# Performance work log

Measured on AMD Instinct MI355X. Metric: run time of the kernel, lower is better.

## Reference

```python
import jax, jax.numpy as jnp
import numpy as np

FP8_MAX = 448.0  # torch.finfo(float8_e4m3fn).max

def _fp8_round(v):
    # round-to-nearest fp8 e4m3fn, back to f32 (simulated quantization)
    return v.astype(jnp.float8_e4m3fn).astype(jnp.float32)

def setup_inputs() -> dict:
    key = jax.random.key(0)
    k_x, k_w, k_b = jax.random.split(key, 3)
    M, K, N = 8, 8192, 8192
    x = jax.random.normal(k_x, (M, K), dtype=jnp.float32)
    w = jax.random.normal(k_w, (K, N), dtype=jnp.float32) * 0.02
    # per-output-column weight quantization (amax-to-scale)
    w_amax = jnp.max(jnp.abs(w), axis=0)                      # [N]
    w_scale = jnp.where(w_amax > 0, FP8_MAX / w_amax, 1.0)    # [N]
    weight_fp8_t = _fp8_round(w * w_scale[None, :])           # [K, N] fp8 values in f32
    weight_scale_inv = (1.0 / w_scale).astype(jnp.float32)    # [N]
    bias = jax.random.normal(k_b, (N,), dtype=jnp.float32) * 0.01
    return {"x": x, "weight_fp8_t": weight_fp8_t,
            "weight_scale_inv": weight_scale_inv, "bias": bias}

def reference(x, weight_fp8_t, weight_scale_inv, bias):
    # dynamic per-row activation quantization: amax -> scale
    amax = jnp.max(jnp.abs(x), axis=-1)                       # [M]
    x_scale = jnp.where(amax > 0, FP8_MAX / amax, 1.0)        # [M]
    x_fp8 = _fp8_round(x * x_scale[:, None])                  # [M, K]
    # scaled matmul: acc * x_scale_inv * weight_scale_inv (per row / per col)
    acc = jnp.einsum('mk,kn->mn', x_fp8, weight_fp8_t)        # [M, N]
    y = acc * (1.0 / x_scale)[:, None] * weight_scale_inv[None, :]
    return y + bias[None, :]
```

## Files before the change

kernel.cpp:

```cpp
#include <hip/hip_runtime.h>
#include <stdint.h>

#define MM 8
#define KK 8192
#define NN 8192
#define KC 256
#define KSPLIT (KK / KC)
#define FP8MAXV 448.0f

typedef float f32x4 __attribute__((ext_vector_type(4)));
typedef float f32x2 __attribute__((ext_vector_type(2)));

#define XQT_OFF 64
#define PART_OFF (XQT_OFF + KK * MM)

__device__ __forceinline__ float fp8_e4m3_round(float v) {
    uint32_t u = __float_as_uint(v);
    uint32_t mag = u & 0x7fffffffu;
    if (mag >= 0x3C800000u) {
        uint32_t lsb = (u >> 20) & 1u;
        uint32_t r = u + 0x0007FFFFu + lsb;
        r &= 0xFFF00000u;
        return __uint_as_float(r);
    }
    return rintf(v * 512.0f) * (1.0f / 512.0f);
}

__global__ __launch_bounds__(256) void prep_kernel(const float* __restrict__ x,
                                                   float* __restrict__ ws) {
    const int m = blockIdx.x;
    const int tid = threadIdx.x;
    const float* row = x + (size_t)m * KK;

    float amax = 0.0f;
    for (int k = tid * 4; k < KK; k += 256 * 4) {
        f32x4 v = *(const f32x4*)(row + k);
        amax = fmaxf(amax, fmaxf(fmaxf(fabsf(v.x), fabsf(v.y)),
                                 fmaxf(fabsf(v.z), fabsf(v.w))));
    }
#pragma unroll
    for (int off = 32; off >= 1; off >>= 1)
        amax = fmaxf(amax, __shfl_xor(amax, off, 64));

    __shared__ float sred[4];
    __shared__ float sscale;
    if ((tid & 63) == 0) sred[tid >> 6] = amax;
    __syncthreads();
    if (tid == 0) {
        float a = fmaxf(fmaxf(sred[0], sred[1]), fmaxf(sred[2], sred[3]));
        float scale = (a > 0.0f) ? (FP8MAXV / a) : 1.0f;
        sscale = scale;
        ws[m] = 1.0f / scale;
    }
    __syncthreads();
    const float scale = sscale;

    float* xqT = ws + XQT_OFF;
    for (int k = tid; k < KK; k += 256)
        xqT[(size_t)k * MM + m] = fp8_e4m3_round(row[k] * scale);
}

__global__ __launch_bounds__(256, 4) void gemm_partial(const float* __restrict__ W,
                                                       const float* __restrict__ wsinv,
                                                       const float* __restrict__ ws,
                                                       float* __restrict__ part) {
    const int n  = blockIdx.x * 256 + threadIdx.x;
    const int c  = blockIdx.y;
    const int k0 = c * KC;

    __shared__ float sxq[KC * MM];
    {
        const f32x4* src = (const f32x4*)(ws + XQT_OFF + (size_t)k0 * MM);
        ((f32x4*)sxq)[threadIdx.x]       = src[threadIdx.x];
        ((f32x4*)sxq)[threadIdx.x + 256] = src[threadIdx.x + 256];
    }
    __syncthreads();

    f32x2 acc[4];
#pragma unroll
    for (int i = 0; i < 4; ++i) acc[i] = (f32x2)0.0f;

    const float* Wp = W + (size_t)k0 * NN + n;
#pragma unroll 8
    for (int k = 0; k < KC; ++k) {
        float w = Wp[(size_t)k * NN];
        const f32x2* a2 = (const f32x2*)(sxq + k * MM);
        acc[0] += a2[0] * w;
        acc[1] += a2[1] * w;
        acc[2] += a2[2] * w;
        acc[3] += a2[3] * w;
    }

    const float wsn = wsinv[n];
    float* p = part + ((size_t)c * MM) * NN + n;
#pragma unroll
    for (int i = 0; i < 4; ++i) {
        p[(size_t)(2 * i + 0) * NN] = acc[i].x * (ws[2 * i + 0] * wsn);
        p[(size_t)(2 * i + 1) * NN] = acc[i].y * (ws[2 * i + 1] * wsn);
    }
}

__global__ __launch_bounds__(256) void reduce_kernel(const float* __restrict__ part,
                                                     const float* __restrict__ bias,
                                                     float* __restrict__ out) {
    const int idx = blockIdx.x * 256 + threadIdx.x;
    float s = bias[idx & (NN - 1)];
#pragma unroll
    for (int c = 0; c < KSPLIT; ++c)
        s += part[(size_t)c * MM * NN + idx];
    out[idx] = s;
}

__global__ __launch_bounds__(256) void init_kernel(const float* __restrict__ bias,
                                                   float* __restrict__ out) {
    int idx = blockIdx.x * 256 + threadIdx.x;
    out[idx] = bias[idx & (NN - 1)];
}

__global__ __launch_bounds__(256, 4) void gemm_atomic(const float* __restrict__ W,
                                                      const float* __restrict__ wsinv,
                                                      const float* __restrict__ ws,
                                                      float* __restrict__ out) {
    const int n  = blockIdx.x * 256 + threadIdx.x;
    const int k0 = blockIdx.y * KC;

    __shared__ float sxq[KC * MM];
    {
        const f32x4* src = (const f32x4*)(ws + XQT_OFF + (size_t)k0 * MM);
        ((f32x4*)sxq)[threadIdx.x]       = src[threadIdx.x];
        ((f32x4*)sxq)[threadIdx.x + 256] = src[threadIdx.x + 256];
    }
    __syncthreads();

    f32x2 acc[4];
#pragma unroll
    for (int i = 0; i < 4; ++i) acc[i] = (f32x2)0.0f;

    const float* Wp = W + (size_t)k0 * NN + n;
#pragma unroll 8
    for (int k = 0; k < KC; ++k) {
        float w = Wp[(size_t)k * NN];
        const f32x2* a2 = (const f32x2*)(sxq + k * MM);
        acc[0] += a2[0] * w;
        acc[1] += a2[1] * w;
        acc[2] += a2[2] * w;
        acc[3] += a2[3] * w;
    }

    const float wsn = wsinv[n];
#pragma unroll
    for (int i = 0; i < 4; ++i) {
        unsafeAtomicAdd(out + (size_t)(2 * i + 0) * NN + n, acc[i].x * (ws[2 * i + 0] * wsn));
        unsafeAtomicAdd(out + (size_t)(2 * i + 1) * NN + n, acc[i].y * (ws[2 * i + 1] * wsn));
    }
}

extern "C" void kernel_launch(void* const* d_in, const int* in_sizes, int n_in,
                              void* d_out, int out_size, void* d_ws, size_t ws_size,
                              hipStream_t stream) {
    const float* x     = (const float*)d_in[0];
    const float* W     = (const float*)d_in[1];
    const float* wsinv = (const float*)d_in[2];
    const float* bias  = (const float*)d_in[3];
    float* out = (float*)d_out;
    float* ws  = (float*)d_ws;

    const size_t need = (size_t)(PART_OFF + (size_t)KSPLIT * MM * NN) * sizeof(float);

    prep_kernel<<<MM, 256, 0, stream>>>(x, ws);

    if (ws_size >= need) {
        float* part = ws + PART_OFF;
        gemm_partial<<<dim3(NN / 256, KSPLIT), 256, 0, stream>>>(W, wsinv, ws, part);
        reduce_kernel<<<(MM * NN) / 256, 256, 0, stream>>>(part, bias, out);
    } else {
        init_kernel<<<(MM * NN) / 256, 256, 0, stream>>>(bias, out);
        gemm_atomic<<<dim3(NN / 256, KSPLIT), 256, 0, stream>>>(W, wsinv, ws, out);
    }
}
```

Before: 65.23 us.

## Process two columns per thread with register double-buffered weight loads

Each thread now computes two adjacent output columns using 8-byte vector weight loads. Weight rows are prefetched into two register buffers of 8 rows each, so loads overlap with the FMAs. The shared-memory staging of quantized activations and its barrier are removed; activations are read straight from global memory, where the values are uniform across the wave. The grid is halved and occupancy is lowered to 2 blocks per SIMD. This trades fewer resident waves and a smaller grid (512 blocks) for more memory-level parallelism per thread.

```diff
diff --git a/kernel.cpp b/kernel.cpp
--- a/kernel.cpp
+++ b/kernel.cpp
@@ -6,6 +6,7 @@
 #define NN 8192
 #define KC 256
 #define KSPLIT (KK / KC)
+#define G 8
 #define FP8MAXV 448.0f
 
 typedef float f32x4 __attribute__((ext_vector_type(4)));
@@ -60,44 +61,62 @@
         xqT[(size_t)k * MM + m] = fp8_e4m3_round(row[k] * scale);
 }
 
-__global__ __launch_bounds__(256, 4) void gemm_partial(const float* __restrict__ W,
+__global__ __launch_bounds__(256, 2) void gemm_partial(const float* __restrict__ W,
                                                        const float* __restrict__ wsinv,
                                                        const float* __restrict__ ws,
                                                        float* __restrict__ part) {
-    const int n  = blockIdx.x * 256 + threadIdx.x;
-    const int c  = blockIdx.y;
-    const int k0 = c * KC;
+    const int tid = threadIdx.x;
+    const int n2  = (blockIdx.x * 256 + tid) * 2;
+    const int c   = blockIdx.y;
+    const int k0  = c * KC;
 
-    __shared__ float sxq[KC * MM];
-    {
-        const f32x4* src = (const f32x4*)(ws + XQT_OFF + (size_t)k0 * MM);
-        ((f32x4*)sxq)[threadIdx.x]       = src[threadIdx.x];
-        ((f32x4*)sxq)[threadIdx.x + 256] = src[threadIdx.x + 256];
+    const float* __restrict__ Wp = W + (size_t)k0 * NN + n2;
+    const float* __restrict__ xq = ws + XQT_OFF + (size_t)k0 * MM;
+
+    f32x2 acc[MM];
+#pragma unroll
+    for (int m = 0; m < MM; ++m) acc[m] = (f32x2)0.0f;
+
+    f32x2 wA[G], wB[G];
+
+    auto loadg = [&](f32x2 (&buf)[G], int gbase) {
+#pragma unroll
+        for (int j = 0; j < G; ++j)
+            buf[j] = *(const f32x2*)(Wp + (size_t)(gbase + j) * NN);
+    };
+    auto compute = [&](f32x2 (&buf)[G], int gbase) {
+#pragma unroll
+        for (int j = 0; j < G; ++j) {
+            const float* a = xq + (size_t)(gbase + j) * MM;
+            f32x2 w = buf[j];
+            acc[0] += w * a[0];
+            acc[1] += w * a[1];
+            acc[2] += w * a[2];
+            acc[3] += w * a[3];
+            acc[4] += w * a[4];
+            acc[5] += w * a[5];
+            acc[6] += w * a[6];
+            acc[7] += w * a[7];
+        }
+    };
+
+    loadg(wA, 0 * G);
+    loadg(wB, 1 * G);
+    int g = 0;
+    for (; g + 2 < KC / G; g += 2) {
+        compute(wA, (g + 0) * G);
+        loadg(wA, (g + 2) * G);
+        compute(wB, (g + 1) * G);
+        loadg(wB, (g + 3) * G);
     }
-    __syncthreads();
+    compute(wA, (g + 0) * G);
+    compute(wB, (g + 1) * G);
 
-    f32x2 acc[4];
+    const f32x2 wsn = *(const f32x2*)(wsinv + n2);
+    float* p = part + ((size_t)c * MM) * NN + n2;
 #pragma unroll
-    for (int i = 0; i < 4; ++i) acc[i] = (f32x2)0.0f;
-
-    const float* Wp = W + (size_t)k0 * NN + n;
-#pragma unroll 8
-    for (int k = 0; k < KC; ++k) {
-        float w = Wp[(size_t)k * NN];
-        const f32x2* a2 = (const f32x2*)(sxq + k * MM);
-        acc[0] += a2[0] * w;
-        acc[1] += a2[1] * w;
-        acc[2] += a2[2] * w;
-        acc[3] += a2[3] * w;
-    }
-
-    const float wsn = wsinv[n];
-    float* p = part + ((size_t)c * MM) * NN + n;
-#pragma unroll
-    for (int i = 0; i < 4; ++i) {
-        p[(size_t)(2 * i + 0) * NN] = acc[i].x * (ws[2 * i + 0] * wsn);
-        p[(size_t)(2 * i + 1) * NN] = acc[i].y * (ws[2 * i + 1] * wsn);
-    }
+    for (int m = 0; m < MM; ++m)
+        *(f32x2*)(p + (size_t)m * NN) = acc[m] * (ws[m] * wsn);
 }
 
 __global__ __launch_bounds__(256) void reduce_kernel(const float* __restrict__ part,
@@ -117,41 +136,34 @@
     out[idx] = bias[idx & (NN - 1)];
 }
 
-__global__ __launch_bounds__(256, 4) void gemm_atomic(const float* __restrict__ W,
+__global__ __launch_bounds__(256, 2) void gemm_atomic(const float* __restrict__ W,
                                                       const float* __restrict__ wsinv,
                                                       const float* __restrict__ ws,
                                                       float* __restrict__ out) {
-    const int n  = blockIdx.x * 256 + threadIdx.x;
-    const int k0 = blockIdx.y * KC;
+    const int tid = threadIdx.x;
+    const int n2  = (blockIdx.x * 256 + tid) * 2;
+    const int k0  = blockIdx.y * KC;
 
-    __shared__ float sxq[KC * MM];
-    {
-        const f32x4* src = (const f32x4*)(ws + XQT_OFF + (size_t)k0 * MM);
-        ((f32x4*)sxq)[threadIdx.x]       = src[threadIdx.x];
-        ((f32x4*)sxq)[threadIdx.x + 256] = src[threadIdx.x + 256];
-    }
-    __syncthreads();
+    const float* __restrict__ Wp = W + (size_t)k0 * NN + n2;
+    const float* __restrict__ xq = ws + XQT_OFF + (size_t)k0 * MM;
 
-    f32x2 acc[4];
+    f32x2 acc[MM];
 #pragma unroll
-    for (int i = 0; i < 4; ++i) acc[i] = (f32x2)0.0f;
+    for (int m = 0; m < MM; ++m) acc[m] = (f32x2)0.0f;
 
-    const float* Wp = W + (size_t)k0 * NN + n;
-#pragma unroll 8
     for (int k = 0; k < KC; ++k) {
-        float w = Wp[(size_t)k * NN];
-        const f32x2* a2 = (const f32x2*)(sxq + k * MM);
-        acc[0] += a2[0] * w;
-        acc[1] += a2[1] * w;
-        acc[2] += a2[2] * w;
-        acc[3] += a2[3] * w;
+        f32x2 w = *(const f32x2*)(Wp + (size_t)k * NN);
+        const float* a = xq + (size_t)k * MM;
+#pragma unroll
+        for (int m = 0; m < MM; ++m) acc[m] += w * a[m];
     }
 
-    const float wsn = wsinv[n];
+    const f32x2 wsn = *(const f32x2*)(wsinv + n2);
 #pragma unroll
-    for (int i = 0; i < 4; ++i) {
-        unsafeAtomicAdd(out + (size_t)(2 * i + 0) * NN + n, acc[i].x * (ws[2 * i + 0] * wsn));
-        unsafeAtomicAdd(out + (size_t)(2 * i + 1) * NN + n, acc[i].y * (ws[2 * i + 1] * wsn));
+    for (int m = 0; m < MM; ++m) {
+        f32x2 r = acc[m] * (ws[m] * wsn);
+        unsafeAtomicAdd(out + (size_t)m * NN + n2 + 0, r.x);
+        unsafeAtomicAdd(out + (size_t)m * NN + n2 + 1, r.y);
     }
 }
 
@@ -171,10 +183,10 @@
 
     if (ws_size >= need) {
         float* part = ws + PART_OFF;
-        gemm_partial<<<dim3(NN / 256, KSPLIT), 256, 0, stream>>>(W, wsinv, ws, part);
+        gemm_partial<<<dim3(NN / 512, KSPLIT), 256, 0, stream>>>(W, wsinv, ws, part);
         reduce_kernel<<<(MM * NN) / 256, 256, 0, stream>>>(part, bias, out);
     } else {
         init_kernel<<<(MM * NN) / 256, 256, 0, stream>>>(bias, out);
-        gemm_atomic<<<dim3(NN / 256, KSPLIT), 256, 0, stream>>>(W, wsinv, ws, out);
+        gemm_atomic<<<dim3(NN / 512, KSPLIT), 256, 0, stream>>>(W, wsinv, ws, out);
     }
 }
```

New measurement: 77.64 us. 1.19x slower.
